# Kernel tuning notes

Hardware: AMD Instinct MI355X
Metric: run time of the kernel (lower is better)

The kernel has to match this reference:

```python
import jax, jax.numpy as jnp
import numpy as np

B, TENC, EPROJS, DUNITS, ODIM, L, ATT_DIM = 64, 800, 512, 512, 5000, 128, 320
SOS = EOS = ODIM - 1


def setup_inputs() -> dict:
    key = jax.random.key(0)
    ks = jax.random.split(key, 16)
    s = 0.02
    D = DUNITS
    return {
        "hpad": jax.random.normal(ks[0], (B, TENC, EPROJS), jnp.float32),
        # keep lengths in [TENC//2, TENC] so every row has valid frames
        "hlen": jnp.clip(jax.random.randint(ks[1], (B,), 0, TENC + 1), TENC // 2, TENC).astype(jnp.int32),
        "ys": jax.random.randint(ks[2], (B, L), 0, ODIM - 1),  # int labels (exclude eos)
        "embed": s * jax.random.normal(ks[3], (ODIM, D), jnp.float32),
        # torch.nn.LSTMCell params: gates order (i, f, g, o)
        "W_ih0": s * jax.random.normal(ks[4], (4 * D, D + EPROJS), jnp.float32),
        "W_hh0": s * jax.random.normal(ks[5], (4 * D, D), jnp.float32),
        "b_ih0": jnp.zeros((4 * D,), jnp.float32),
        "b_hh0": jnp.zeros((4 * D,), jnp.float32),
        "W_ih1": s * jax.random.normal(ks[6], (4 * D, D), jnp.float32),
        "W_hh1": s * jax.random.normal(ks[7], (4 * D, D), jnp.float32),
        "b_ih1": jnp.zeros((4 * D,), jnp.float32),
        "b_hh1": jnp.zeros((4 * D,), jnp.float32),
        # AttDot attention projections (no bias, as in espnet mlp_enc/mlp_dec usage)
        "Wa_enc": s * jax.random.normal(ks[8], (EPROJS, ATT_DIM), jnp.float32),
        "Wa_dec": s * jax.random.normal(ks[9], (D, ATT_DIM), jnp.float32),
        "W_out": s * jax.random.normal(ks[10], (ODIM, D), jnp.float32),
        "b_out": jnp.zeros((ODIM,), jnp.float32),
    }


def _lstm_cell(x, h, c, Wi, Wh, bi, bh):
    g = x @ Wi.T + bi + h @ Wh.T + bh
    i, f, gg, o = jnp.split(g, 4, axis=-1)
    c2 = jax.nn.sigmoid(f) * c + jax.nn.sigmoid(i) * jnp.tanh(gg)
    h2 = jax.nn.sigmoid(o) * jnp.tanh(c2)
    return h2, c2


def _forward(hpad, hlen, ys, embed, W_ih0, W_hh0, b_ih0, b_hh0,
             W_ih1, W_hh1, b_ih1, b_hh1, Wa_enc, Wa_dec, W_out, b_out):
    D = DUNITS
    tmask = jnp.arange(TENC)[None, :] < hlen[:, None]          # [B, T]
    hm = hpad * tmask[:, :, None]                               # mask_by_length
    enc_pre = jnp.tanh(jnp.einsum('bte,ea->bta', hm, Wa_enc))   # [B, T, A] precomputed

    sos_col = jnp.full((B, 1), SOS, ys.dtype)
    eos_col = jnp.full((B, 1), EOS, ys.dtype)
    ys_in = jnp.concatenate([sos_col, ys], axis=1)              # [B, L+1]
    ys_out = jnp.concatenate([ys, eos_col], axis=1)             # [B, L+1]
    eys = embed[ys_in]                                          # [B, L+1, D]

    zeros = jnp.zeros((B, D), hpad.dtype)
    carry0 = (zeros, zeros, zeros, zeros)  # z0, c0, z1, c1

    def step(carry, ey_t):
        z0, c0, z1, c1 = carry
        # AttDot: e = <tanh(enc W), tanh(z0 W)> with length masking
        d = jnp.tanh(z0 @ Wa_dec)                               # [B, A]
        e = jnp.einsum('ba,bta->bt', d, enc_pre)                # [B, T]
        e = jnp.where(tmask, e, jnp.float32(-1e9))
        w = jax.nn.softmax(e, axis=-1)
        att_c = jnp.einsum('bt,bte->be', w, hm)                 # [B, eprojs]
        x = jnp.concatenate([ey_t, att_c], axis=-1)             # [B, D+eprojs]
        z0, c0 = _lstm_cell(x, z0, c0, W_ih0, W_hh0, b_ih0, b_hh0)
        z1, c1 = _lstm_cell(z0, z1, c1, W_ih1, W_hh1, b_ih1, b_hh1)
        return (z0, c0, z1, c1), z1                             # gen_feat='s' -> top hidden

    _, z_all = jax.lax.scan(step, carry0, jnp.swapaxes(eys, 0, 1))  # [L+1, B, D]
    z_all = jnp.swapaxes(z_all, 0, 1)                           # [B, L+1, D]

    logits = jnp.einsum('bld,vd->blv', z_all, W_out) + b_out    # [B, L+1, V]
    logp = jax.nn.log_softmax(logits, axis=-1)
    nll = -jnp.take_along_axis(logp, ys_out[..., None], axis=-1)[..., 0]
    # F.cross_entropy mean over all tokens (no padding here), then *= mean(len(ys_in)) - 1 = L
    loss = nll.mean() * jnp.float32(L)
    acc = (logits.argmax(-1) == ys_out).mean()
    return loss, acc


def reference(hpad, hlen, ys, embed, W_ih0, W_hh0, b_ih0, b_hh0,
              W_ih1, W_hh1, b_ih1, b_hh1, Wa_enc, Wa_dec, W_out, b_out):
    return _forward(hpad, hlen, ys, embed, W_ih0, W_hh0, b_ih0, b_hh0,
                    W_ih1, W_hh1, b_ih1, b_hh1, Wa_enc, Wa_dec, W_out, b_out)
```

## Files before the change

kernel.cpp:

```cpp
#include <hip/hip_runtime.h>
#include <math.h>

typedef unsigned short u16;
typedef unsigned char u8;
typedef float f32x4 __attribute__((ext_vector_type(4)));
typedef short s16x8 __attribute__((ext_vector_type(8)));

#define ODIM 5000
#define NROWS 8256

__device__ inline u16 f2bf(float f){
  unsigned u = __float_as_uint(f);
  return (u16)((u + 0x7FFFu + ((u >> 16) & 1u)) >> 16);
}
__device__ inline float bf2f(u16 h){ return __uint_as_float(((unsigned)h) << 16); }
__device__ inline float sigm(float x){ return 1.f/(1.f + expf(-x)); }

__device__ inline unsigned f2fp8(float f){
  unsigned u = __float_as_uint(f);
  unsigned s = (u>>24)&0x80u;
  int e = (int)((u>>23)&0xffu) - 127;
  if (e < -7) return s;
  unsigned full = (u & 0x7fffffu) | 0x800000u;
  unsigned keep = full >> 20;
  unsigned rem  = full & 0xFFFFFu;
  keep += (rem > 0x80000u) || (rem == 0x80000u && (keep & 1u));
  int te = e + 7;
  if (keep >= 16u){ keep >>= 1; te += 1; }
  if (te >= 16) return s | 0x7Eu;
  if (te < 1)  return s;
  return s | ((unsigned)te<<3) | (keep & 7u);
}
__device__ inline float fp8d(unsigned v){
  unsigned r = ((v & 0x80u) << 24) | (((v & 0x7fu) + 960u) << 20);
  return __uint_as_float(r);
}

__global__ void a0_init(float* att2, float* dz, float* z0f, float* z1f,
                        float* c0, float* c1, float* accum){
  int tid = blockIdx.x*256 + threadIdx.x, n = 64*256;
  for (int i=tid;i<2*64*516;i+=n) att2[i]=0.f;
  for (int i=tid;i<10240;i+=n) dz[i]=0.f;
  for (int i=tid;i<32768;i+=n){ z0f[i]=0.f; z1f[i]=0.f; c0[i]=0.f; c1[i]=0.f; }
  if (tid < 8) accum[tid]=0.f;
}

__global__ void a1_wcvt(const float* waenc, const float* wadec,
  const float* wih0, const float* whh0, const float* wih1, const float* whh1,
  const float* bih0, const float* bhh0, const float* bih1, const float* bhh1,
  const float* wout,
  u16* waencT, u16* wadecT, u16* wcat0, u16* wcat1, u16* wee, u16* woutb,
  float* bc0, float* bc1)
{
  int tid = blockIdx.x*blockDim.x + threadIdx.x;
  int nth = gridDim.x*blockDim.x;
  for (int i=tid; i<320*512; i+=nth){
    int n=i>>9, k=i&511;
    waencT[i] = f2bf(waenc[k*320+n]);
    wadecT[i] = f2bf(wadec[k*320+n]);
  }
  for (int i=tid; i<2048*1024; i+=nth){
    int np=i>>10, k=i&1023;
    int u=np>>2, g=np&3, r=g*512+u;
    wcat0[i] = f2bf(k<512 ? wih0[r*1024+512+k] : whh0[r*512+(k-512)]);
    wcat1[i] = f2bf(k<512 ? wih1[r*512+k]      : whh1[r*512+(k-512)]);
  }
  for (int i=tid; i<2048*512; i+=nth){
    int np=i>>9, k=i&511;
    int u=np>>2, g=np&3, r=g*512+u;
    wee[i] = f2bf(wih0[r*1024+k]);
  }
  for (int i=tid; i<5000*512; i+=nth) woutb[i] = f2bf(wout[i]);
  for (int i=tid; i<2048; i+=nth){
    int u=i>>2, g=i&3, r=g*512+u;
    bc0[i] = bih0[r]+bhh0[r];
    bc1[i] = bih1[r]+bhh1[r];
  }
}

__global__ __launch_bounds__(256) void a2_encpre(
  const float* __restrict__ hpad, const int* __restrict__ hlen,
  const u16* __restrict__ waencT, u8* __restrict__ hm8, u8* __restrict__ encp8)
{
  __shared__ u16 A[64][40];
  __shared__ u16 BT[320][40];
  int tid = threadIdx.x, blk = blockIdx.x;
  int wave = tid>>6, lane = tid&63;
  f32x4 acc[20];
  #pragma unroll
  for (int f=0;f<20;f++) acc[f] = (f32x4){0.f,0.f,0.f,0.f};
  int srow = tid>>2, skoff = (tid&3)*8;
  int grow_s = blk*64 + srow;
  int b_s = grow_s/800, t_s = grow_s - b_s*800;
  bool valid_s = t_s < hlen[b_s];
  for (int c=0;c<16;c++){
    int k0 = c*32;
    {
      const float* src = hpad + (size_t)grow_s*512 + k0 + skoff;
      float4 v0 = *(const float4*)(src);
      float4 v1 = *(const float4*)(src+4);
      if (!valid_s){ v0 = make_float4(0,0,0,0); v1 = make_float4(0,0,0,0); }
      *(short4*)&A[srow][skoff] = make_short4(
        (short)f2bf(v0.x),(short)f2bf(v0.y),(short)f2bf(v0.z),(short)f2bf(v0.w));
      *(short4*)&A[srow][skoff+4] = make_short4(
        (short)f2bf(v1.x),(short)f2bf(v1.y),(short)f2bf(v1.z),(short)f2bf(v1.w));
      unsigned lo = f2fp8(v0.x) | (f2fp8(v0.y)<<8) | (f2fp8(v0.z)<<16) | (f2fp8(v0.w)<<24);
      unsigned hi = f2fp8(v1.x) | (f2fp8(v1.y)<<8) | (f2fp8(v1.z)<<16) | (f2fp8(v1.w)<<24);
      *(uint2*)(hm8 + (size_t)grow_s*512 + k0 + skoff) = make_uint2(lo, hi);
    }
    for (int id=tid; id<1280; id+=256){
      int n = id>>2, kv = (id&3)*8;
      *(s16x8*)&BT[n][kv] = *(const s16x8*)(waencT + n*512 + k0 + kv);
    }
    __syncthreads();
    s16x8 av = *(const s16x8*)&A[wave*16 + (lane&15)][(lane>>4)*8];
    #pragma unroll
    for (int f=0;f<20;f++){
      s16x8 bv = *(const s16x8*)&BT[f*16+(lane&15)][(lane>>4)*8];
      acc[f] = __builtin_amdgcn_mfma_f32_16x16x32_bf16(av,bv,acc[f],0,0,0);
    }
    __syncthreads();
  }
  #pragma unroll
  for (int f=0;f<20;f++){
    int col = f*16 + (lane&15);
    #pragma unroll
    for (int r=0;r<4;r++){
      int grow = blk*64 + wave*16 + (lane>>4)*4 + r;
      encp8[(size_t)grow*320 + col] = (u8)f2fp8(tanhf(acc[f][r]));
    }
  }
}

__global__ __launch_bounds__(256) void a3_geys(
  const int* __restrict__ ys, const float* __restrict__ embed,
  const u16* __restrict__ wee, const float* __restrict__ bc0,
  u16* __restrict__ geys)
{
  __shared__ u16 A[64][88];
  __shared__ u16 BT[256][88];
  int t = blockIdx.x, nt = blockIdx.y, tid = threadIdx.x;
  int wave=tid>>6, lane=tid&63;
  f32x4 acc[16];
  #pragma unroll
  for (int f=0;f<16;f++) acc[f]=(f32x4){0.f,0.f,0.f,0.f};
  int srow = tid>>2, skoff=(tid&3)*16;
  int idx = (t==0) ? (ODIM-1) : ys[srow*128 + (t-1)];
  const float* asrc = embed + (size_t)idx*512;
  for (int c=0;c<8;c++){
    int k0=c*64;
    #pragma unroll
    for (int i=0;i<16;i+=4){
      float4 v = *(const float4*)(asrc + k0 + skoff + i);
      *(short4*)&A[srow][skoff+i] =
        make_short4((short)f2bf(v.x),(short)f2bf(v.y),(short)f2bf(v.z),(short)f2bf(v.w));
    }
    for (int id=tid; id<2048; id+=256){
      int n = id>>3, kv=(id&7)*8;
      *(s16x8*)&BT[n][kv] = *(const s16x8*)(wee + (size_t)(nt*256+n)*512 + k0 + kv);
    }
    __syncthreads();
    #pragma unroll
    for (int kk=0;kk<64;kk+=32){
      s16x8 av = *(const s16x8*)&A[wave*16+(lane&15)][kk+(lane>>4)*8];
      #pragma unroll
      for (int f=0;f<16;f++){
        s16x8 bv = *(const s16x8*)&BT[f*16+(lane&15)][kk+(lane>>4)*8];
        acc[f] = __builtin_amdgcn_mfma_f32_16x16x32_bf16(av,bv,acc[f],0,0,0);
      }
    }
    __syncthreads();
  }
  #pragma unroll
  for (int f=0;f<16;f++){
    int colL = f*16+(lane&15);
    int gc = nt*256+colL;
    float bb = bc0[gc];
    #pragma unroll
    for (int r=0;r<4;r++){
      int row = wave*16 + (lane>>4)*4 + r;
      geys[(size_t)(t*64+row)*2048 + gc] = f2bf(acc[f][r] + bb);
    }
  }
}

__global__ __launch_bounds__(256) void k1_att(
  const u16* __restrict__ d_g, const u8* __restrict__ encp8,
  const u8* __restrict__ hm8, const int* __restrict__ hlen,
  float* __restrict__ att)
{
  int b = blockIdx.x >> 3, ch = blockIdx.x & 7;
  int wave = threadIdx.x >> 6, lane = threadIdx.x & 63;
  int len = hlen[b];
  float dreg[8];
  {
    s16x8 dv = 0;
    if (lane < 40) dv = *(const s16x8*)(d_g + b*320 + lane*8);
    #pragma unroll
    for (int j=0;j<8;j++) dreg[j] = bf2f((u16)dv[j]);
  }
  float attacc[8];
  #pragma unroll
  for (int j=0;j<8;j++) attacc[j]=0.f;
  float sacc = 0.f;
  int t0 = ch*100;
  int tend = t0+100 < len ? t0+100 : len;
  for (int i0 = t0 + wave; i0 < tend; i0 += 16){
    uint2 ea[4], ha[4];
    #pragma unroll
    for (int q=0;q<4;q++){
      int tt = i0 + 4*q;
      if (tt < tend){
        if (lane<40) ea[q] = *(const uint2*)(encp8 + (size_t)(b*800+tt)*320 + lane*8);
        ha[q] = *(const uint2*)(hm8 + (size_t)(b*800+tt)*512 + lane*8);
      }
    }
    #pragma unroll
    for (int q=0;q<4;q++){
      int tt = i0 + 4*q;
      if (tt < tend){
        float e = 0.f;
        if (lane<40){
          unsigned w0 = ea[q].x, w1 = ea[q].y;
          e += dreg[0]*fp8d(w0&0xffu) + dreg[1]*fp8d((w0>>8)&0xffu)
             + dreg[2]*fp8d((w0>>16)&0xffu) + dreg[3]*fp8d(w0>>24);
          e += dreg[4]*fp8d(w1&0xffu) + dreg[5]*fp8d((w1>>8)&0xffu)
             + dreg[6]*fp8d((w1>>16)&0xffu) + dreg[7]*fp8d(w1>>24);
        }
        #pragma unroll
        for (int off=32; off; off>>=1) e += __shfl_xor(e, off);
        float pw = expf(fminf(e, 60.f));
        sacc += pw;
        unsigned h0 = ha[q].x, h1 = ha[q].y;
        attacc[0] += pw*fp8d(h0&0xffu);
        attacc[1] += pw*fp8d((h0>>8)&0xffu);
        attacc[2] += pw*fp8d((h0>>16)&0xffu);
        attacc[3] += pw*fp8d(h0>>24);
        attacc[4] += pw*fp8d(h1&0xffu);
        attacc[5] += pw*fp8d((h1>>8)&0xffu);
        attacc[6] += pw*fp8d((h1>>16)&0xffu);
        attacc[7] += pw*fp8d(h1>>24);
      }
    }
  }
  __shared__ float attl[4][512];
  __shared__ float sl[4];
  #pragma unroll
  for (int j=0;j<8;j++) attl[wave][lane*8+j] = attacc[j];
  if (lane==0) sl[wave] = sacc;
  __syncthreads();
  for (int c = threadIdx.x; c < 512; c += 256){
    float v = attl[0][c]+attl[1][c]+attl[2][c]+attl[3][c];
    atomicAdd(&att[b*516 + c], v);
  }
  if (threadIdx.x==0) atomicAdd(&att[b*516 + 512], sl[0]+sl[1]+sl[2]+sl[3]);
}

__global__ __launch_bounds__(256) void k2_cell0(
  const float* __restrict__ attp, float* __restrict__ attz,
  const u16* __restrict__ z0p, u16* __restrict__ z0n,
  float* __restrict__ c0,
  const u16* __restrict__ wcat0, const u16* __restrict__ geyt)
{
  __shared__ __align__(16) char smem[16896];
  __shared__ float sinv[64];
  u16 (*A)[88]  = (u16(*)[88])smem;
  u16 (*BT)[88] = (u16(*)[88])(smem+11264);
  int tid = threadIdx.x, nb = blockIdx.x;
  int wave=tid>>6, lane=tid&63;
  if (tid < 64) sinv[tid] = 1.f/attp[tid*516+512];
  __syncthreads();
  f32x4 acc[2];
  acc[0]=(f32x4){0.f,0.f,0.f,0.f}; acc[1]=(f32x4){0.f,0.f,0.f,0.f};
  int srow=tid>>2, skoff=(tid&3)*16;
  int brow=tid>>3, bkoff=(tid&7)*8;
  for (int c=0;c<16;c++){
    int k0=c*64;
    if (c<8){
      const float* src = attp + srow*516 + k0 + skoff;
      float sv = sinv[srow];
      #pragma unroll
      for (int i=0;i<16;i+=4){
        float4 v = *(const float4*)(src+i);
        *(short4*)&A[srow][skoff+i] = make_short4(
          (short)f2bf(v.x*sv),(short)f2bf(v.y*sv),(short)f2bf(v.z*sv),(short)f2bf(v.w*sv));
      }
    } else {
      const u16* src = z0p + srow*512 + (k0-512) + skoff;
      *(s16x8*)&A[srow][skoff]   = *(const s16x8*)(src);
      *(s16x8*)&A[srow][skoff+8] = *(const s16x8*)(src+8);
    }
    *(s16x8*)&BT[brow][bkoff] = *(const s16x8*)(wcat0 + (size_t)(nb*32+brow)*1024 + k0 + bkoff);
    __syncthreads();
    #pragma unroll
    for (int kk=0;kk<64;kk+=32){
      s16x8 av = *(const s16x8*)&A[wave*16+(lane&15)][kk+(lane>>4)*8];
      #pragma unroll
      for (int f=0;f<2;f++){
        s16x8 bv = *(const s16x8*)&BT[f*16+(lane&15)][kk+(lane>>4)*8];
        acc[f] = __builtin_amdgcn_mfma_f32_16x16x32_bf16(av,bv,acc[f],0,0,0);
      }
    }
    __syncthreads();
  }
  float (*gl)[36] = (float(*)[36])smem;
  #pragma unroll
  for (int f=0;f<2;f++){
    int colL = f*16+(lane&15);
    #pragma unroll
    for (int r=0;r<4;r++){
      int rowL = wave*16+(lane>>4)*4+r;
      gl[rowL][colL] = acc[f][r] + bf2f(geyt[rowL*2048 + nb*32 + colL]);
    }
  }
  __syncthreads();
  for (int it=tid; it<512; it+=256){
    int bb=it>>3, ul=it&7;
    float gi=gl[bb][ul*4], gf=gl[bb][ul*4+1], gg=gl[bb][ul*4+2], go=gl[bb][ul*4+3];
    int ug = nb*8+ul;
    float cp = c0[bb*512+ug];
    float cn = sigm(gf)*cp + sigm(gi)*tanhf(gg);
    float z = sigm(go)*tanhf(cn);
    c0[bb*512+ug]=cn;
    z0n[bb*512+ug]=f2bf(z);
  }
  for (int i=tid + nb*256; i < 64*516; i += 64*256) attz[i] = 0.f;
}

__global__ __launch_bounds__(256) void k3_cell1(
  const u16* __restrict__ z0n, const u16* __restrict__ z1p,
  u16* __restrict__ z1n, float* __restrict__ c1,
  const u16* __restrict__ wcat1, const float* __restrict__ bc1,
  u16* __restrict__ zallt,
  const u16* __restrict__ wadecT, u16* __restrict__ d_g)
{
  __shared__ __align__(16) char smem[25600];
  int tid = threadIdx.x, wave=tid>>6, lane=tid&63;
  int blk = blockIdx.x;
  u16 (*A)[88]  = (u16(*)[88])smem;
  if (blk < 64){
    u16 (*BT)[88] = (u16(*)[88])(smem+11264);
    int nb = blk;
    f32x4 acc[2];
    acc[0]=(f32x4){0.f,0.f,0.f,0.f}; acc[1]=(f32x4){0.f,0.f,0.f,0.f};
    int srow=tid>>2, skoff=(tid&3)*16;
    int brow=tid>>3, bkoff=(tid&7)*8;
    for (int c=0;c<16;c++){
      int k0=c*64;
      const u16* asrc = (c<8) ? (z0n + srow*512 + k0 + skoff)
                              : (z1p + srow*512 + (k0-512) + skoff);
      *(s16x8*)&A[srow][skoff]   = *(const s16x8*)asrc;
      *(s16x8*)&A[srow][skoff+8] = *(const s16x8*)(asrc+8);
      *(s16x8*)&BT[brow][bkoff] = *(const s16x8*)(wcat1 + (size_t)(nb*32+brow)*1024 + k0 + bkoff);
      __syncthreads();
      #pragma unroll
      for (int kk=0;kk<64;kk+=32){
        s16x8 av = *(const s16x8*)&A[wave*16+(lane&15)][kk+(lane>>4)*8];
        #pragma unroll
        for (int f=0;f<2;f++){
          s16x8 bv = *(const s16x8*)&BT[f*16+(lane&15)][kk+(lane>>4)*8];
          acc[f] = __builtin_amdgcn_mfma_f32_16x16x32_bf16(av,bv,acc[f],0,0,0);
        }
      }
      __syncthreads();
    }
    float (*gl)[36] = (float(*)[36])smem;
    #pragma unroll
    for (int f=0;f<2;f++){
      int colL = f*16+(lane&15);
      float bb = bc1[nb*32+colL];
      #pragma unroll
      for (int r=0;r<4;r++){
        int rowL = wave*16+(lane>>4)*4+r;
        gl[rowL][colL] = acc[f][r] + bb;
      }
    }
    __syncthreads();
    for (int it=tid; it<512; it+=256){
      int bb=it>>3, ul=it&7;
      float gi=gl[bb][ul*4], gf=gl[bb][ul*4+1], gg=gl[bb][ul*4+2], go=gl[bb][ul*4+3];
      int ug = nb*8+ul;
      float cp = c1[bb*512+ug];
      float cn = sigm(gf)*cp + sigm(gi)*tanhf(gg);
      float z = sigm(go)*tanhf(cn);
      c1[bb*512+ug]=cn;
      u16 zb = f2bf(z);
      z1n[bb*512+ug]=zb;
      zallt[bb*512+ug]=zb;
    }
  } else {
    u16 (*BT)[88] = (u16(*)[88])(smem+11264);
    int nb = blk-64;
    f32x4 acc[5];
    #pragma unroll
    for (int f=0;f<5;f++) acc[f]=(f32x4){0.f,0.f,0.f,0.f};
    int srow=tid>>2, skoff=(tid&3)*16;
    for (int c=0;c<8;c++){
      int k0=c*64;
      const u16* asrc = z0n + srow*512 + k0 + skoff;
      *(s16x8*)&A[srow][skoff]   = *(const s16x8*)asrc;
      *(s16x8*)&A[srow][skoff+8] = *(const s16x8*)(asrc+8);
      for (int id=tid; id<640; id+=256){
        int n=id>>3, kv=(id&7)*8;
        *(s16x8*)&BT[n][kv] = *(const s16x8*)(wadecT + (size_t)(nb*80+n)*512 + k0 + kv);
      }
      __syncthreads();
      #pragma unroll
      for (int kk=0;kk<64;kk+=32){
        s16x8 av = *(const s16x8*)&A[wave*16+(lane&15)][kk+(lane>>4)*8];
        #pragma unroll
        for (int f=0;f<5;f++){
          s16x8 bv = *(const s16x8*)&BT[f*16+(lane&15)][kk+(lane>>4)*8];
          acc[f] = __builtin_amdgcn_mfma_f32_16x16x32_bf16(av,bv,acc[f],0,0,0);
        }
      }
      __syncthreads();
    }
    #pragma unroll
    for (int f=0;f<5;f++){
      int col = nb*80 + f*16 + (lane&15);
      #pragma unroll
      for (int r=0;r<4;r++){
        int row = wave*16 + (lane>>4)*4 + r;
        d_g[row*320+col] = f2bf(tanhf(acc[f][r]));
      }
    }
  }
}

__global__ __launch_bounds__(512) void k4_logits(
  const u16* __restrict__ zall, const u16* __restrict__ woutb,
  const float* __restrict__ b_out, const int* __restrict__ ys,
  float* __restrict__ partials)
{
  __shared__ char smem[46080];
  u16 (*A)[40]  = (u16(*)[40])smem;
  u16 (*BT)[40] = (u16(*)[40])(smem + 5120);
  int t = blockIdx.x, v = blockIdx.y;
  int tid = threadIdx.x, wave = tid>>6, lane = tid&63;
  int mf = wave>>1;
  int nh = (wave&1)*256;
  f32x4 acc[16];
  #pragma unroll
  for (int f=0;f<16;f++) acc[f]=(f32x4){0.f,0.f,0.f,0.f};
  for (int c=0;c<16;c++){
    int k0 = c*32;
    { int row = tid>>3, koff=(tid&7)*4;
      *(short4*)&A[row][koff] = *(const short4*)(zall + (size_t)(t*64+row)*512 + k0 + koff); }
    { int n = v*512 + tid;
      if (n < ODIM){
        const u16* src = woutb + (size_t)n*512 + k0;
        #pragma unroll
        for (int i=0;i<32;i+=8) *(s16x8*)&BT[tid][i] = *(const s16x8*)(src+i);
      } else {
        s16x8 z = 0;
        #pragma unroll
        for (int i=0;i<32;i+=8) *(s16x8*)&BT[tid][i] = z;
      }
    }
    __syncthreads();
    s16x8 av = *(const s16x8*)&A[mf*16 + (lane&15)][(lane>>4)*8];
    #pragma unroll
    for (int f=0;f<16;f++){
      s16x8 bv = *(const s16x8*)&BT[nh + f*16 + (lane&15)][(lane>>4)*8];
      acc[f] = __builtin_amdgcn_mfma_f32_16x16x32_bf16(av,bv,acc[f],0,0,0);
    }
    __syncthreads();
  }
  float (*ll)[518] = (float(*)[518])smem;
  for (int g=0; g<4; g++){
    if (mf == g){
      #pragma unroll
      for (int f=0;f<16;f++){
        int colL = nh + f*16 + (lane&15);
        int gcol = v*512 + colL;
        float bo = (gcol < ODIM) ? b_out[gcol] : 0.f;
        #pragma unroll
        for (int r=0;r<4;r++){
          int rowL = (lane>>4)*4 + r;
          ll[rowL][colL] = acc[f][r] + bo;
        }
      }
    }
    __syncthreads();
    int r = tid>>5, j = tid&31;
    float m = -1e30f, s = 0.f, amax = -1e30f; int aidx = 0;
    #pragma unroll
    for (int i=0;i<16;i++){
      int cL = j + 32*i;
      int gc = v*512 + cL;
      if (gc < ODIM){
        float val = ll[r][cL];
        if (val > m){ s = s*expf(m-val) + 1.f; m = val; }
        else s += expf(val - m);
        if (val > amax){ amax = val; aidx = gc; }
      }
    }
    #pragma unroll
    for (int off=16; off; off>>=1){
      float mo = __shfl_xor(m, off), so = __shfl_xor(s, off);
      float ao = __shfl_xor(amax, off); int io = __shfl_xor(aidx, off);
      float M = fmaxf(m, mo);
      s = s*expf(m-M) + so*expf(mo-M);
      m = M;
      if (ao > amax || (ao == amax && io < aidx)){ amax = ao; aidx = io; }
    }
    if (j == 0){
      int b = g*16 + r;
      int grow = t*64 + b;
      int lab = (t < 128) ? ys[b*128 + t] : (ODIM-1);
      float labval = 0.f, labf = 0.f;
      int lo = lab - v*512;
      if (lo >= 0 && lo < 512){ labval = ll[r][lo]; labf = 1.f; }
      float* pp = partials + (size_t)(grow*10 + v)*8;
      pp[0]=m; pp[1]=s; pp[2]=amax; pp[3]=__int_as_float(aidx); pp[4]=labval; pp[5]=labf;
    }
    __syncthreads();
  }
}

__global__ __launch_bounds__(256) void k5_loss(
  const float* __restrict__ partials, const int* __restrict__ ys, float* accum)
{
  int row = blockIdx.x*256 + threadIdx.x;
  float nll = 0.f; int corr = 0;
  if (row < NROWS){
    float M=-1e30f, S=0.f, amax=-1e30f, labval=0.f; int aidx=0;
    for (int v=0;v<10;v++){
      const float* pp = partials + (size_t)(row*10+v)*8;
      float m=pp[0], s=pp[1], a=pp[2]; int ai=__float_as_int(pp[3]);
      float MM = fmaxf(M, m);
      S = S*expf(M-MM) + s*expf(m-MM);
      M = MM;
      if (a > amax || (a == amax && ai < aidx)){ amax=a; aidx=ai; }
      if (pp[5] != 0.f) labval = pp[4];
    }
    nll = M + logf(S) - labval;
    int t = row>>6, b = row&63;
    int lab = (t < 128) ? ys[b*128+t] : (ODIM-1);
    corr = (aidx == lab) ? 1 : 0;
  }
  __shared__ float sn[256]; __shared__ int sc[256];
  sn[threadIdx.x]=nll; sc[threadIdx.x]=corr; __syncthreads();
  for (int st=128; st; st>>=1){
    if (threadIdx.x<st){ sn[threadIdx.x]+=sn[threadIdx.x+st]; sc[threadIdx.x]+=sc[threadIdx.x+st]; }
    __syncthreads();
  }
  if (threadIdx.x==0){
    atomicAdd(accum, sn[0]);
    atomicAdd((int*)accum + 1, sc[0]);
  }
}

__global__ void k6_final(const float* accum, float* out){
  out[0] = accum[0]/(float)NROWS * 128.f;
  out[1] = (float)(((const int*)accum)[1])/(float)NROWS;
}

extern "C" void kernel_launch(void* const* d_in, const int* in_sizes, int n_in,
                              void* d_out, int out_size, void* d_ws, size_t ws_size,
                              hipStream_t stream)
{
  const float* hpad  = (const float*)d_in[0];
  const int*   hlen  = (const int*)d_in[1];
  const int*   ys    = (const int*)d_in[2];
  const float* embed = (const float*)d_in[3];
  const float* wih0  = (const float*)d_in[4];
  const float* whh0  = (const float*)d_in[5];
  const float* bih0  = (const float*)d_in[6];
  const float* bhh0  = (const float*)d_in[7];
  const float* wih1  = (const float*)d_in[8];
  const float* whh1  = (const float*)d_in[9];
  const float* bih1  = (const float*)d_in[10];
  const float* bhh1  = (const float*)d_in[11];
  const float* waenc = (const float*)d_in[12];
  const float* wadec = (const float*)d_in[13];
  const float* wout  = (const float*)d_in[14];
  const float* bout  = (const float*)d_in[15];

  char* ws = (char*)d_ws;
  u8*    hm8     = (u8*)(ws + 0);
  u8*    encp8   = (u8*)(ws + 26214400);
  u16*   waencT  = (u16*)(ws + 42598400);
  u16*   wadecT  = (u16*)(ws + 42926080);
  u16*   wcat0   = (u16*)(ws + 43253760);
  u16*   wcat1   = (u16*)(ws + 47448064);
  u16*   wee     = (u16*)(ws + 51642368);
  u16*   woutb   = (u16*)(ws + 53739520);
  float* bc0     = (float*)(ws + 58859520);
  float* bc1     = (float*)(ws + 58867712);
  u16*   geys    = (u16*)(ws + 58875904);
  u16*   d_g     = (u16*)(ws + 92692480);
  float* att     = (float*)(ws + 92733440);
  u16*   z0b     = (u16*)(ws + 92997632);
  u16*   z1b     = (u16*)(ws + 93128704);
  float* c0      = (float*)(ws + 93259776);
  float* c1      = (float*)(ws + 93390848);
  u16*   zall    = (u16*)(ws + 93521920);
  float* partials= (float*)(ws + 101976064);
  float* accum   = (float*)(ws + 104617984);

  a0_init<<<64,256,0,stream>>>(att, (float*)d_g, (float*)z0b, (float*)z1b, c0, c1, accum);
  a1_wcvt<<<512,256,0,stream>>>(waenc, wadec, wih0, whh0, wih1, whh1,
                                bih0, bhh0, bih1, bhh1, wout,
                                waencT, wadecT, wcat0, wcat1, wee, woutb, bc0, bc1);
  a2_encpre<<<800,256,0,stream>>>(hpad, hlen, waencT, hm8, encp8);
  a3_geys<<<dim3(129,8),256,0,stream>>>(ys, embed, wee, bc0, geys);

  for (int t=0; t<129; t++){
    int p = t & 1;
    k1_att<<<512,256,0,stream>>>(d_g, encp8, hm8, hlen, att + p*64*516);
    k2_cell0<<<64,256,0,stream>>>(att + p*64*516, att + (p^1)*64*516,
                                  z0b + (p^1)*64*512, z0b + p*64*512,
                                  c0, wcat0, geys + (size_t)t*64*2048);
    k3_cell1<<<68,256,0,stream>>>(z0b + p*64*512, z1b + (p^1)*64*512,
                                  z1b + p*64*512, c1, wcat1, bc1,
                                  zall + (size_t)t*64*512, wadecT, d_g);
  }

  k4_logits<<<dim3(129,10),512,0,stream>>>(zall, woutb, bout, ys, partials);
  k5_loss<<<33,256,0,stream>>>(partials, ys, accum);
  k6_final<<<1,1,0,stream>>>(accum, (float*)d_out);
}
```

Baseline: 7.018 ms.

## Fold decoder attention projection into cell0 and overlap cell1 with attention

The per-step decoder attention projection is no longer a separate GEMM inside the cell1 kernel. Each cell0 block now writes the partial product of its slice of z0 times Wa_dec to a buffer, and the attention kernel sums those partials and applies tanh. Cell1 for step t-1 runs in extra blocks of the step-t attention kernel, which cuts the per-step launches from three to two and lets cell1 overlap attention. In exchange, each step writes and rereads a 64x64x320 float partial buffer, and a final cell1 launch is added after the loop.

```diff
diff --git a/kernel.cpp b/kernel.cpp
--- a/kernel.cpp
+++ b/kernel.cpp
@@ -36,11 +36,11 @@
   return __uint_as_float(r);
 }
 
-__global__ void a0_init(float* att2, float* dz, float* z0f, float* z1f,
+__global__ void a0_init(float* att2, float* pd, float* z0f, float* z1f,
                         float* c0, float* c1, float* accum){
   int tid = blockIdx.x*256 + threadIdx.x, n = 64*256;
   for (int i=tid;i<2*64*516;i+=n) att2[i]=0.f;
-  for (int i=tid;i<10240;i+=n) dz[i]=0.f;
+  for (int i=tid;i<2621440;i+=n) pd[i]=0.f;
   for (int i=tid;i<32768;i+=n){ z0f[i]=0.f; z1f[i]=0.f; c0[i]=0.f; c1[i]=0.f; }
   if (tid < 8) accum[tid]=0.f;
 }
@@ -49,7 +49,7 @@
   const float* wih0, const float* whh0, const float* wih1, const float* whh1,
   const float* bih0, const float* bhh0, const float* bih1, const float* bhh1,
   const float* wout,
-  u16* waencT, u16* wadecT, u16* wcat0, u16* wcat1, u16* wee, u16* woutb,
+  u16* waencT, u16* wdKC, u16* wcat0, u16* wcat1, u16* wee, u16* woutb,
   float* bc0, float* bc1)
 {
   int tid = blockIdx.x*blockDim.x + threadIdx.x;
@@ -57,7 +57,7 @@
   for (int i=tid; i<320*512; i+=nth){
     int n=i>>9, k=i&511;
     waencT[i] = f2bf(waenc[k*320+n]);
-    wadecT[i] = f2bf(wadec[k*320+n]);
+    wdKC[i]   = f2bf(wadec[i]);
   }
   for (int i=tid; i<2048*1024; i+=nth){
     int np=i>>10, k=i&1023;
@@ -184,163 +184,112 @@
   }
 }
 
-__global__ __launch_bounds__(256) void k1_att(
-  const u16* __restrict__ d_g, const u8* __restrict__ encp8,
-  const u8* __restrict__ hm8, const int* __restrict__ hlen,
-  float* __restrict__ att)
-{
-  int b = blockIdx.x >> 3, ch = blockIdx.x & 7;
-  int wave = threadIdx.x >> 6, lane = threadIdx.x & 63;
-  int len = hlen[b];
-  float dreg[8];
-  {
-    s16x8 dv = 0;
-    if (lane < 40) dv = *(const s16x8*)(d_g + b*320 + lane*8);
-    #pragma unroll
-    for (int j=0;j<8;j++) dreg[j] = bf2f((u16)dv[j]);
-  }
-  float attacc[8];
-  #pragma unroll
-  for (int j=0;j<8;j++) attacc[j]=0.f;
-  float sacc = 0.f;
-  int t0 = ch*100;
-  int tend = t0+100 < len ? t0+100 : len;
-  for (int i0 = t0 + wave; i0 < tend; i0 += 16){
-    uint2 ea[4], ha[4];
-    #pragma unroll
-    for (int q=0;q<4;q++){
-      int tt = i0 + 4*q;
-      if (tt < tend){
-        if (lane<40) ea[q] = *(const uint2*)(encp8 + (size_t)(b*800+tt)*320 + lane*8);
-        ha[q] = *(const uint2*)(hm8 + (size_t)(b*800+tt)*512 + lane*8);
-      }
-    }
-    #pragma unroll
-    for (int q=0;q<4;q++){
-      int tt = i0 + 4*q;
-      if (tt < tend){
-        float e = 0.f;
-        if (lane<40){
-          unsigned w0 = ea[q].x, w1 = ea[q].y;
-          e += dreg[0]*fp8d(w0&0xffu) + dreg[1]*fp8d((w0>>8)&0xffu)
-             + dreg[2]*fp8d((w0>>16)&0xffu) + dreg[3]*fp8d(w0>>24);
-          e += dreg[4]*fp8d(w1&0xffu) + dreg[5]*fp8d((w1>>8)&0xffu)
-             + dreg[6]*fp8d((w1>>16)&0xffu) + dreg[7]*fp8d(w1>>24);
+__global__ __launch_bounds__(256) void k1p(
+  int t,
+  const u8* __restrict__ encp8, const u8* __restrict__ hm8, const int* __restrict__ hlen,
+  const float* __restrict__ pd,
+  const u16* __restrict__ wcat1, const float* __restrict__ bc1,
+  const u16* __restrict__ z0b, u16* __restrict__ z1b, float* __restrict__ c1,
+  u16* __restrict__ zall, float* __restrict__ att)
+{
+  __shared__ __align__(16) char smem[25600];
+  const int blk = blockIdx.x, tid = threadIdx.x;
+  const int wave = tid>>6, lane = tid&63;
+  const int p2 = (t+1)&1;
+
+  if (blk < 512){
+    int b = blk>>3, ch = blk&7;
+    float* attp = att + ((t&1)*64*516);
+    float* attl = (float*)smem;
+    float* sl   = (float*)(smem+8192);
+    float* dl   = (float*)(smem+8224);
+    {
+      const float* q0 = pd + (size_t)p2*1310720 + (size_t)b*320;
+      for (int col=tid; col<320; col+=256){
+        const float* q = q0 + col;
+        float a0=0.f,a1=0.f,a2=0.f,a3=0.f,a4=0.f,a5=0.f,a6=0.f,a7=0.f;
+        #pragma unroll
+        for (int s=0;s<64;s+=8){
+          a0 += q[(size_t)(s+0)*20480];
+          a1 += q[(size_t)(s+1)*20480];
+          a2 += q[(size_t)(s+2)*20480];
+          a3 += q[(size_t)(s+3)*20480];
+          a4 += q[(size_t)(s+4)*20480];
+          a5 += q[(size_t)(s+5)*20480];
+          a6 += q[(size_t)(s+6)*20480];
+          a7 += q[(size_t)(s+7)*20480];
         }
-        #pragma unroll
-        for (int off=32; off; off>>=1) e += __shfl_xor(e, off);
-        float pw = expf(fminf(e, 60.f));
-        sacc += pw;
-        unsigned h0 = ha[q].x, h1 = ha[q].y;
-        attacc[0] += pw*fp8d(h0&0xffu);
-        attacc[1] += pw*fp8d((h0>>8)&0xffu);
-        attacc[2] += pw*fp8d((h0>>16)&0xffu);
-        attacc[3] += pw*fp8d(h0>>24);
-        attacc[4] += pw*fp8d(h1&0xffu);
-        attacc[5] += pw*fp8d((h1>>8)&0xffu);
-        attacc[6] += pw*fp8d((h1>>16)&0xffu);
-        attacc[7] += pw*fp8d(h1>>24);
-      }
-    }
-  }
-  __shared__ float attl[4][512];
-  __shared__ float sl[4];
-  #pragma unroll
-  for (int j=0;j<8;j++) attl[wave][lane*8+j] = attacc[j];
-  if (lane==0) sl[wave] = sacc;
-  __syncthreads();
-  for (int c = threadIdx.x; c < 512; c += 256){
-    float v = attl[0][c]+attl[1][c]+attl[2][c]+attl[3][c];
-    atomicAdd(&att[b*516 + c], v);
-  }
-  if (threadIdx.x==0) atomicAdd(&att[b*516 + 512], sl[0]+sl[1]+sl[2]+sl[3]);
-}
-
-__global__ __launch_bounds__(256) void k2_cell0(
-  const float* __restrict__ attp, float* __restrict__ attz,
-  const u16* __restrict__ z0p, u16* __restrict__ z0n,
-  float* __restrict__ c0,
-  const u16* __restrict__ wcat0, const u16* __restrict__ geyt)
-{
-  __shared__ __align__(16) char smem[16896];
-  __shared__ float sinv[64];
-  u16 (*A)[88]  = (u16(*)[88])smem;
-  u16 (*BT)[88] = (u16(*)[88])(smem+11264);
-  int tid = threadIdx.x, nb = blockIdx.x;
-  int wave=tid>>6, lane=tid&63;
-  if (tid < 64) sinv[tid] = 1.f/attp[tid*516+512];
-  __syncthreads();
-  f32x4 acc[2];
-  acc[0]=(f32x4){0.f,0.f,0.f,0.f}; acc[1]=(f32x4){0.f,0.f,0.f,0.f};
-  int srow=tid>>2, skoff=(tid&3)*16;
-  int brow=tid>>3, bkoff=(tid&7)*8;
-  for (int c=0;c<16;c++){
-    int k0=c*64;
-    if (c<8){
-      const float* src = attp + srow*516 + k0 + skoff;
-      float sv = sinv[srow];
-      #pragma unroll
-      for (int i=0;i<16;i+=4){
-        float4 v = *(const float4*)(src+i);
-        *(short4*)&A[srow][skoff+i] = make_short4(
-          (short)f2bf(v.x*sv),(short)f2bf(v.y*sv),(short)f2bf(v.z*sv),(short)f2bf(v.w*sv));
-      }
-    } else {
-      const u16* src = z0p + srow*512 + (k0-512) + skoff;
-      *(s16x8*)&A[srow][skoff]   = *(const s16x8*)(src);
-      *(s16x8*)&A[srow][skoff+8] = *(const s16x8*)(src+8);
-    }
-    *(s16x8*)&BT[brow][bkoff] = *(const s16x8*)(wcat0 + (size_t)(nb*32+brow)*1024 + k0 + bkoff);
-    __syncthreads();
-    #pragma unroll
-    for (int kk=0;kk<64;kk+=32){
-      s16x8 av = *(const s16x8*)&A[wave*16+(lane&15)][kk+(lane>>4)*8];
-      #pragma unroll
-      for (int f=0;f<2;f++){
-        s16x8 bv = *(const s16x8*)&BT[f*16+(lane&15)][kk+(lane>>4)*8];
-        acc[f] = __builtin_amdgcn_mfma_f32_16x16x32_bf16(av,bv,acc[f],0,0,0);
-      }
-    }
-    __syncthreads();
-  }
-  float (*gl)[36] = (float(*)[36])smem;
-  #pragma unroll
-  for (int f=0;f<2;f++){
-    int colL = f*16+(lane&15);
-    #pragma unroll
-    for (int r=0;r<4;r++){
-      int rowL = wave*16+(lane>>4)*4+r;
-      gl[rowL][colL] = acc[f][r] + bf2f(geyt[rowL*2048 + nb*32 + colL]);
-    }
-  }
-  __syncthreads();
-  for (int it=tid; it<512; it+=256){
-    int bb=it>>3, ul=it&7;
-    float gi=gl[bb][ul*4], gf=gl[bb][ul*4+1], gg=gl[bb][ul*4+2], go=gl[bb][ul*4+3];
-    int ug = nb*8+ul;
-    float cp = c0[bb*512+ug];
-    float cn = sigm(gf)*cp + sigm(gi)*tanhf(gg);
-    float z = sigm(go)*tanhf(cn);
-    c0[bb*512+ug]=cn;
-    z0n[bb*512+ug]=f2bf(z);
-  }
-  for (int i=tid + nb*256; i < 64*516; i += 64*256) attz[i] = 0.f;
-}
-
-__global__ __launch_bounds__(256) void k3_cell1(
-  const u16* __restrict__ z0n, const u16* __restrict__ z1p,
-  u16* __restrict__ z1n, float* __restrict__ c1,
-  const u16* __restrict__ wcat1, const float* __restrict__ bc1,
-  u16* __restrict__ zallt,
-  const u16* __restrict__ wadecT, u16* __restrict__ d_g)
-{
-  __shared__ __align__(16) char smem[25600];
-  int tid = threadIdx.x, wave=tid>>6, lane=tid&63;
-  int blk = blockIdx.x;
-  u16 (*A)[88]  = (u16(*)[88])smem;
-  if (blk < 64){
+        dl[col] = tanhf(((a0+a1)+(a2+a3))+((a4+a5)+(a6+a7)));
+      }
+    }
+    __syncthreads();
+    float dreg[8];
+    #pragma unroll
+    for (int j=0;j<8;j++) dreg[j] = (lane<40) ? dl[lane*8+j] : 0.f;
+    float attacc[8];
+    #pragma unroll
+    for (int j=0;j<8;j++) attacc[j]=0.f;
+    float sacc = 0.f;
+    int len = hlen[b];
+    int t0 = ch*100;
+    int tend = t0+100 < len ? t0+100 : len;
+    for (int i0 = t0 + wave; i0 < tend; i0 += 16){
+      uint2 ea[4], ha[4];
+      #pragma unroll
+      for (int q=0;q<4;q++){
+        int tt = i0 + 4*q;
+        if (tt < tend){
+          if (lane<40) ea[q] = *(const uint2*)(encp8 + (size_t)(b*800+tt)*320 + lane*8);
+          ha[q] = *(const uint2*)(hm8 + (size_t)(b*800+tt)*512 + lane*8);
+        }
+      }
+      #pragma unroll
+      for (int q=0;q<4;q++){
+        int tt = i0 + 4*q;
+        if (tt < tend){
+          float e = 0.f;
+          if (lane<40){
+            unsigned w0 = ea[q].x, w1 = ea[q].y;
+            e += dreg[0]*fp8d(w0&0xffu) + dreg[1]*fp8d((w0>>8)&0xffu)
+               + dreg[2]*fp8d((w0>>16)&0xffu) + dreg[3]*fp8d(w0>>24);
+            e += dreg[4]*fp8d(w1&0xffu) + dreg[5]*fp8d((w1>>8)&0xffu)
+               + dreg[6]*fp8d((w1>>16)&0xffu) + dreg[7]*fp8d(w1>>24);
+          }
+          #pragma unroll
+          for (int off=32; off; off>>=1) e += __shfl_xor(e, off);
+          float pw = expf(fminf(e, 60.f));
+          sacc += pw;
+          unsigned h0 = ha[q].x, h1 = ha[q].y;
+          attacc[0] += pw*fp8d(h0&0xffu);
+          attacc[1] += pw*fp8d((h0>>8)&0xffu);
+          attacc[2] += pw*fp8d((h0>>16)&0xffu);
+          attacc[3] += pw*fp8d(h0>>24);
+          attacc[4] += pw*fp8d(h1&0xffu);
+          attacc[5] += pw*fp8d((h1>>8)&0xffu);
+          attacc[6] += pw*fp8d((h1>>16)&0xffu);
+          attacc[7] += pw*fp8d(h1>>24);
+        }
+      }
+    }
+    __syncthreads();
+    #pragma unroll
+    for (int j=0;j<8;j++) attl[wave*512 + lane*8+j] = attacc[j];
+    if (lane==0) sl[wave] = sacc;
+    __syncthreads();
+    for (int c2 = tid; c2 < 512; c2 += 256){
+      float v = attl[c2]+attl[512+c2]+attl[1024+c2]+attl[1536+c2];
+      atomicAdd(&attp[b*516 + c2], v);
+    }
+    if (tid==0) atomicAdd(&attp[b*516 + 512], sl[0]+sl[1]+sl[2]+sl[3]);
+  } else {
+    if (t < 1) return;
+    int nb = blk - 512;
+    const u16* z0n = z0b + p2*64*512;
+    const u16* z1p = z1b + ((p2^1)*64*512);
+    u16* z1n = z1b + p2*64*512;
+    u16* zallt = zall + (size_t)(t-1)*64*512;
+    u16 (*A)[88]  = (u16(*)[88])smem;
     u16 (*BT)[88] = (u16(*)[88])(smem+11264);
-    int nb = blk;
     f32x4 acc[2];
     acc[0]=(f32x4){0.f,0.f,0.f,0.f}; acc[1]=(f32x4){0.f,0.f,0.f,0.f};
     int srow=tid>>2, skoff=(tid&3)*16;
@@ -388,43 +337,152 @@
       z1n[bb*512+ug]=zb;
       zallt[bb*512+ug]=zb;
     }
-  } else {
-    u16 (*BT)[88] = (u16(*)[88])(smem+11264);
-    int nb = blk-64;
-    f32x4 acc[5];
-    #pragma unroll
-    for (int f=0;f<5;f++) acc[f]=(f32x4){0.f,0.f,0.f,0.f};
-    int srow=tid>>2, skoff=(tid&3)*16;
-    for (int c=0;c<8;c++){
-      int k0=c*64;
-      const u16* asrc = z0n + srow*512 + k0 + skoff;
-      *(s16x8*)&A[srow][skoff]   = *(const s16x8*)asrc;
-      *(s16x8*)&A[srow][skoff+8] = *(const s16x8*)(asrc+8);
-      for (int id=tid; id<640; id+=256){
-        int n=id>>3, kv=(id&7)*8;
-        *(s16x8*)&BT[n][kv] = *(const s16x8*)(wadecT + (size_t)(nb*80+n)*512 + k0 + kv);
-      }
-      __syncthreads();
-      #pragma unroll
-      for (int kk=0;kk<64;kk+=32){
-        s16x8 av = *(const s16x8*)&A[wave*16+(lane&15)][kk+(lane>>4)*8];
-        #pragma unroll
-        for (int f=0;f<5;f++){
-          s16x8 bv = *(const s16x8*)&BT[f*16+(lane&15)][kk+(lane>>4)*8];
-          acc[f] = __builtin_amdgcn_mfma_f32_16x16x32_bf16(av,bv,acc[f],0,0,0);
-        }
-      }
-      __syncthreads();
-    }
-    #pragma unroll
-    for (int f=0;f<5;f++){
-      int col = nb*80 + f*16 + (lane&15);
-      #pragma unroll
-      for (int r=0;r<4;r++){
-        int row = wave*16 + (lane>>4)*4 + r;
-        d_g[row*320+col] = f2bf(tanhf(acc[f][r]));
-      }
-    }
+  }
+}
+
+__global__ __launch_bounds__(256) void k2p(
+  const float* __restrict__ attp, float* __restrict__ attz,
+  const u16* __restrict__ z0p, u16* __restrict__ z0n,
+  float* __restrict__ c0,
+  const u16* __restrict__ wcat0, const u16* __restrict__ geyt,
+  const u16* __restrict__ wdKC, float* __restrict__ pdout)
+{
+  __shared__ __align__(16) char smem[16896];
+  __shared__ float sinv[64];
+  __shared__ float zsl[512];
+  __shared__ u16 wsl[2560];
+  u16 (*A)[88]  = (u16(*)[88])smem;
+  u16 (*BT)[88] = (u16(*)[88])(smem+11264);
+  int tid = threadIdx.x, nb = blockIdx.x;
+  int wave=tid>>6, lane=tid&63;
+  if (tid < 64) sinv[tid] = 1.f/attp[tid*516+512];
+  for (int id=tid; id<320; id+=256)
+    *(s16x8*)&wsl[id*8] = *(const s16x8*)(wdKC + nb*2560 + id*8);
+  __syncthreads();
+  f32x4 acc[2];
+  acc[0]=(f32x4){0.f,0.f,0.f,0.f}; acc[1]=(f32x4){0.f,0.f,0.f,0.f};
+  int srow=tid>>2, skoff=(tid&3)*16;
+  int brow=tid>>3, bkoff=(tid&7)*8;
+  for (int c=0;c<16;c++){
+    int k0=c*64;
+    if (c<8){
+      const float* src = attp + srow*516 + k0 + skoff;
+      float sv = sinv[srow];
+      #pragma unroll
+      for (int i=0;i<16;i+=4){
+        float4 v = *(const float4*)(src+i);
+        *(short4*)&A[srow][skoff+i] = make_short4(
+          (short)f2bf(v.x*sv),(short)f2bf(v.y*sv),(short)f2bf(v.z*sv),(short)f2bf(v.w*sv));
+      }
+    } else {
+      const u16* src = z0p + srow*512 + (k0-512) + skoff;
+      *(s16x8*)&A[srow][skoff]   = *(const s16x8*)(src);
+      *(s16x8*)&A[srow][skoff+8] = *(const s16x8*)(src+8);
+    }
+    *(s16x8*)&BT[brow][bkoff] = *(const s16x8*)(wcat0 + (size_t)(nb*32+brow)*1024 + k0 + bkoff);
+    __syncthreads();
+    #pragma unroll
+    for (int kk=0;kk<64;kk+=32){
+      s16x8 av = *(const s16x8*)&A[wave*16+(lane&15)][kk+(lane>>4)*8];
+      #pragma unroll
+      for (int f=0;f<2;f++){
+        s16x8 bv = *(const s16x8*)&BT[f*16+(lane&15)][kk+(lane>>4)*8];
+        acc[f] = __builtin_amdgcn_mfma_f32_16x16x32_bf16(av,bv,acc[f],0,0,0);
+      }
+    }
+    __syncthreads();
+  }
+  float (*gl)[36] = (float(*)[36])smem;
+  #pragma unroll
+  for (int f=0;f<2;f++){
+    int colL = f*16+(lane&15);
+    #pragma unroll
+    for (int r=0;r<4;r++){
+      int rowL = wave*16+(lane>>4)*4+r;
+      gl[rowL][colL] = acc[f][r] + bf2f(geyt[rowL*2048 + nb*32 + colL]);
+    }
+  }
+  __syncthreads();
+  for (int it=tid; it<512; it+=256){
+    int bb=it>>3, ul=it&7;
+    float gi=gl[bb][ul*4], gf=gl[bb][ul*4+1], gg=gl[bb][ul*4+2], go=gl[bb][ul*4+3];
+    int ug = nb*8+ul;
+    float cp = c0[bb*512+ug];
+    float cn = sigm(gf)*cp + sigm(gi)*tanhf(gg);
+    float z = sigm(go)*tanhf(cn);
+    c0[bb*512+ug]=cn;
+    z0n[bb*512+ug]=f2bf(z);
+    zsl[it] = z;
+  }
+  __syncthreads();
+  for (int idx=tid; idx<20480; idx+=256){
+    int b = idx/320, col = idx - b*320;
+    float a = 0.f;
+    #pragma unroll
+    for (int ul=0; ul<8; ul++)
+      a += zsl[b*8+ul]*bf2f(wsl[ul*320+col]);
+    pdout[(size_t)nb*20480 + idx] = a;
+  }
+  for (int i=tid + nb*256; i < 64*516; i += 64*256) attz[i] = 0.f;
+}
+
+__global__ __launch_bounds__(256) void kf_cell1(
+  const u16* __restrict__ z0n, const u16* __restrict__ z1p,
+  u16* __restrict__ z1n, float* __restrict__ c1,
+  const u16* __restrict__ wcat1, const float* __restrict__ bc1,
+  u16* __restrict__ zallt)
+{
+  __shared__ __align__(16) char smem[25600];
+  int tid = threadIdx.x, wave=tid>>6, lane=tid&63;
+  int nb = blockIdx.x;
+  u16 (*A)[88]  = (u16(*)[88])smem;
+  u16 (*BT)[88] = (u16(*)[88])(smem+11264);
+  f32x4 acc[2];
+  acc[0]=(f32x4){0.f,0.f,0.f,0.f}; acc[1]=(f32x4){0.f,0.f,0.f,0.f};
+  int srow=tid>>2, skoff=(tid&3)*16;
+  int brow=tid>>3, bkoff=(tid&7)*8;
+  for (int c=0;c<16;c++){
+    int k0=c*64;
+    const u16* asrc = (c<8) ? (z0n + srow*512 + k0 + skoff)
+                            : (z1p + srow*512 + (k0-512) + skoff);
+    *(s16x8*)&A[srow][skoff]   = *(const s16x8*)asrc;
+    *(s16x8*)&A[srow][skoff+8] = *(const s16x8*)(asrc+8);
+    *(s16x8*)&BT[brow][bkoff] = *(const s16x8*)(wcat1 + (size_t)(nb*32+brow)*1024 + k0 + bkoff);
+    __syncthreads();
+    #pragma unroll
+    for (int kk=0;kk<64;kk+=32){
+      s16x8 av = *(const s16x8*)&A[wave*16+(lane&15)][kk+(lane>>4)*8];
+      #pragma unroll
+      for (int f=0;f<2;f++){
+        s16x8 bv = *(const s16x8*)&BT[f*16+(lane&15)][kk+(lane>>4)*8];
+        acc[f] = __builtin_amdgcn_mfma_f32_16x16x32_bf16(av,bv,acc[f],0,0,0);
+      }
+    }
+    __syncthreads();
+  }
+  float (*gl)[36] = (float(*)[36])smem;
+  #pragma unroll
+  for (int f=0;f<2;f++){
+    int colL = f*16+(lane&15);
+    float bb = bc1[nb*32+colL];
+    #pragma unroll
+    for (int r=0;r<4;r++){
+      int rowL = wave*16+(lane>>4)*4+r;
+      gl[rowL][colL] = acc[f][r] + bb;
+    }
+  }
+  __syncthreads();
+  for (int it=tid; it<512; it+=256){
+    int bb=it>>3, ul=it&7;
+    float gi=gl[bb][ul*4], gf=gl[bb][ul*4+1], gg=gl[bb][ul*4+2], go=gl[bb][ul*4+3];
+    int ug = nb*8+ul;
+    float cp = c1[bb*512+ug];
+    float cn = sigm(gf)*cp + sigm(gi)*tanhf(gg);
+    float z = sigm(go)*tanhf(cn);
+    c1[bb*512+ug]=cn;
+    u16 zb = f2bf(z);
+    z1n[bb*512+ug]=zb;
+    zallt[bb*512+ug]=zb;
   }
 }
 
@@ -582,7 +640,7 @@
   u8*    hm8     = (u8*)(ws + 0);
   u8*    encp8   = (u8*)(ws + 26214400);
   u16*   waencT  = (u16*)(ws + 42598400);
-  u16*   wadecT  = (u16*)(ws + 42926080);
+  u16*   wdKC    = (u16*)(ws + 42926080);
   u16*   wcat0   = (u16*)(ws + 43253760);
   u16*   wcat1   = (u16*)(ws + 47448064);
   u16*   wee     = (u16*)(ws + 51642368);
@@ -590,33 +648,34 @@
   float* bc0     = (float*)(ws + 58859520);
   float* bc1     = (float*)(ws + 58867712);
   u16*   geys    = (u16*)(ws + 58875904);
-  u16*   d_g     = (u16*)(ws + 92692480);
-  float* att     = (float*)(ws + 92733440);
-  u16*   z0b     = (u16*)(ws + 92997632);
-  u16*   z1b     = (u16*)(ws + 93128704);
-  float* c0      = (float*)(ws + 93259776);
-  float* c1      = (float*)(ws + 93390848);
-  u16*   zall    = (u16*)(ws + 93521920);
-  float* partials= (float*)(ws + 101976064);
-  float* accum   = (float*)(ws + 104617984);
-
-  a0_init<<<64,256,0,stream>>>(att, (float*)d_g, (float*)z0b, (float*)z1b, c0, c1, accum);
+  float* pd      = (float*)(ws + 92692480);
+  float* att     = (float*)(ws + 103178240);
+  u16*   z0b     = (u16*)(ws + 103442432);
+  u16*   z1b     = (u16*)(ws + 103573504);
+  float* c0      = (float*)(ws + 103704576);
+  float* c1      = (float*)(ws + 103835648);
+  u16*   zall    = (u16*)(ws + 103966720);
+  float* partials= (float*)(ws + 112420864);
+  float* accum   = (float*)(ws + 115062784);
+
+  a0_init<<<64,256,0,stream>>>(att, pd, (float*)z0b, (float*)z1b, c0, c1, accum);
   a1_wcvt<<<512,256,0,stream>>>(waenc, wadec, wih0, whh0, wih1, whh1,
                                 bih0, bhh0, bih1, bhh1, wout,
-                                waencT, wadecT, wcat0, wcat1, wee, woutb, bc0, bc1);
+                                waencT, wdKC, wcat0, wcat1, wee, woutb, bc0, bc1);
   a2_encpre<<<800,256,0,stream>>>(hpad, hlen, waencT, hm8, encp8);
   a3_geys<<<dim3(129,8),256,0,stream>>>(ys, embed, wee, bc0, geys);
 
   for (int t=0; t<129; t++){
-    int p = t & 1;
-    k1_att<<<512,256,0,stream>>>(d_g, encp8, hm8, hlen, att + p*64*516);
-    k2_cell0<<<64,256,0,stream>>>(att + p*64*516, att + (p^1)*64*516,
-                                  z0b + (p^1)*64*512, z0b + p*64*512,
-                                  c0, wcat0, geys + (size_t)t*64*2048);
-    k3_cell1<<<68,256,0,stream>>>(z0b + p*64*512, z1b + (p^1)*64*512,
-                                  z1b + p*64*512, c1, wcat1, bc1,
-                                  zall + (size_t)t*64*512, wadecT, d_g);
-  }
+    int p = t & 1, q = p^1;
+    k1p<<<576,256,0,stream>>>(t, encp8, hm8, hlen, pd, wcat1, bc1,
+                              z0b, z1b, c1, zall, att);
+    k2p<<<64,256,0,stream>>>(att + p*64*516, att + q*64*516,
+                             z0b + q*64*512, z0b + p*64*512,
+                             c0, wcat0, geys + (size_t)t*64*2048,
+                             wdKC, pd + (size_t)p*1310720);
+  }
+  kf_cell1<<<64,256,0,stream>>>(z0b, z1b + 64*512, z1b, c1, wcat1, bc1,
+                                zall + (size_t)128*64*512);
 
   k4_logits<<<dim3(129,10),512,0,stream>>>(zall, woutb, bout, ys, partials);
   k5_loss<<<33,256,0,stream>>>(partials, ys, accum);
```

Measured after the change: 7.775 ms. 1.11x slower.
